# Kernel optimization log

Measured on AMD Instinct MI355X. Metric: run time of the kernel, lower is better.

Reference implementation:

```python
import jax, jax.numpy as jnp
import numpy as np

B, C, D, H = 2, 1024, 1024, 16
DH = D // H
EPS = 1e-8


def setup_inputs() -> dict:
    key = jax.random.key(0)
    ks = jax.random.split(key, 12)
    s = 0.02
    return {
        "x": jax.random.normal(ks[0], (B, C, D), dtype=jnp.float32),
        "rms_w": jnp.ones((C, D), dtype=jnp.float32),
        "rms_b": jnp.zeros((C, D), dtype=jnp.float32),
        "Wqkv": jax.random.normal(ks[1], (3 * D, D), dtype=jnp.float32) * s,
        "Wout": jax.random.normal(ks[2], (D, D), dtype=jnp.float32) * s,
        "bout": jnp.zeros((D,), dtype=jnp.float32),
        "Wf": jax.random.normal(ks[3], (D, D), dtype=jnp.float32) * s,
        "bf": jnp.zeros((D,), dtype=jnp.float32),
        "Ww": jax.random.normal(ks[4], (D, D), dtype=jnp.float32) * s,
        "bw": jnp.zeros((D,), dtype=jnp.float32),
        "Wv": jax.random.normal(ks[5], (D, D), dtype=jnp.float32) * s,
        "bv": jnp.zeros((D,), dtype=jnp.float32),
        "beta": jnp.ones((1,), dtype=jnp.float32),
    }


def _rope_cos_sin(C, dh):
    # faithful to source: theta = 10000 ** (-2*(i-1)/dh), i in [0, dh//2)
    i = jnp.arange(dh // 2, dtype=jnp.float32)
    theta = 10000.0 ** (-2.0 * (i - 1.0) / dh)            # [dh//2]
    ang = jnp.arange(C, dtype=jnp.float32)[:, None] * theta  # [C, dh//2]
    return jnp.cos(ang), jnp.sin(ang)


def _rotate(t, cos, sin):
    # equivalent to einsum('bhci,cij->bhcj', t, R) with the source R
    ev, od = t[..., 0::2], t[..., 1::2]          # [B,H,C,dh//2]
    out_ev = ev * cos + od * sin
    out_od = -ev * sin + od * cos
    return jnp.stack([out_ev, out_od], axis=-1).reshape(t.shape)


def _rmsnorm(x, w, b):
    rms = jnp.sqrt(jnp.mean(x * x, axis=-1, keepdims=True) + EPS)
    return w * (x / rms) + b


def _attention(x, Wqkv, Wout, bout):
    qkv = x @ Wqkv.T                               # [B,C,3D]
    q, k, v = jnp.split(qkv, 3, axis=-1)
    def heads(t):
        return t.reshape(B, C, H, DH).transpose(0, 2, 1, 3)  # [B,H,C,dh]
    q, k, v = heads(q), heads(k), heads(v)
    cos, sin = _rope_cos_sin(C, DH)
    qr = _rotate(q, cos, sin)
    kr = _rotate(k, cos, sin)
    scale = 1.0 / jnp.sqrt(jnp.float32(DH))
    num = jnp.exp(jnp.einsum('bhid,bhjd->bhij', qr, kr) * scale)
    den = jnp.sum(jnp.exp(jnp.einsum('bhid,bhjd->bhij', q, k) * scale),
                  axis=-1, keepdims=True)
    attn = num / den
    mask = jnp.tril(jnp.ones((C, C), dtype=bool))
    attn = jnp.where(mask[None, None], attn, 0.0)
    y = attn @ v                                   # [B,H,C,dh]
    y = y.transpose(0, 2, 1, 3).reshape(B, C, D)
    return y @ Wout.T + bout


def _ffn(x, Wf, bf, Ww, bw, Wv, bv, beta):
    h = x @ Wf.T + bf
    wx = h @ Ww.T + bw
    swish = wx * jax.nn.sigmoid(beta * wx)
    return swish * (h @ Wv.T + bv)


def reference(x, rms_w, rms_b, Wqkv, Wout, bout, Wf, bf, Ww, bw, Wv, bv, beta):
    # dropout p is identity in eval mode
    x = _rmsnorm(x, rms_w, rms_b)
    x = x + _attention(x, Wqkv, Wout, bout)
    x = _rmsnorm(x, rms_w, rms_b)   # same shared RMSNorm module applied twice
    x = x + _ffn(x, Wf, bf, Ww, bw, Wv, bv, beta)
    return x
```

## Files before the change

### kernel.cpp

```cpp
#include <hip/hip_runtime.h>
#include <math.h>

#define B_ 2
#define C_ 1024
#define D_ 1024
#define H_ 16
#define DH_ 64
#define EPSF 1e-8f
#define BK 32

typedef __bf16 bf16;
typedef __attribute__((ext_vector_type(4))) __bf16 bf16x4;
typedef __attribute__((ext_vector_type(8))) __bf16 bf16x8;
typedef __attribute__((ext_vector_type(4))) float f32x4;

__device__ inline f32x4 mfma16(bf16x8 a, bf16x8 b, f32x4 c) {
  return __builtin_amdgcn_mfma_f32_16x16x32_bf16(a, b, c, 0, 0, 0);
}

__device__ inline void async16(const bf16* g, bf16* l) {
  __builtin_amdgcn_global_load_lds((const __attribute__((address_space(1))) void*)g,
                                   (__attribute__((address_space(3))) void*)l, 16, 0, 0);
}

__global__ __launch_bounds__(256) void cvt_all_kernel(const float* __restrict__ wqkv,
                                                      const float* __restrict__ wout,
                                                      const float* __restrict__ wf,
                                                      const float* __restrict__ www,
                                                      const float* __restrict__ wv,
                                                      bf16* __restrict__ dst) {
  int seg = blockIdx.x >> 10;
  int local = (blockIdx.x & 1023) * 1024 + threadIdx.x * 4;
  const float* src = seg < 3 ? wqkv + (size_t)seg * (D_ * D_)
                   : seg == 3 ? wout : seg == 4 ? wf : seg == 5 ? www : wv;
  float4 v = *(const float4*)(src + local);
  bf16x4 o;
  o[0] = (bf16)v.x; o[1] = (bf16)v.y; o[2] = (bf16)v.z; o[3] = (bf16)v.w;
  *(bf16x4*)(dst + (size_t)seg * (D_ * D_) + local) = o;
}

__global__ __launch_bounds__(256) void rmsnorm_f32_kernel(const float* __restrict__ x,
                                                          const float* __restrict__ w,
                                                          const float* __restrict__ b,
                                                          bf16* __restrict__ out) {
  int row = blockIdx.x;
  int c = row & (C_ - 1);
  int t = threadIdx.x;
  float4 xv = *(const float4*)(x + (size_t)row * D_ + t * 4);
  float ss = xv.x * xv.x + xv.y * xv.y + xv.z * xv.z + xv.w * xv.w;
#pragma unroll
  for (int m = 1; m < 64; m <<= 1) ss += __shfl_xor(ss, m, 64);
  __shared__ float red[4];
  if ((t & 63) == 0) red[t >> 6] = ss;
  __syncthreads();
  float tot = red[0] + red[1] + red[2] + red[3];
  float inv = rsqrtf(tot * (1.0f / D_) + EPSF);
  float4 wv = *(const float4*)(w + (size_t)c * D_ + t * 4);
  float4 bv = *(const float4*)(b + (size_t)c * D_ + t * 4);
  bf16x4 ov;
  ov[0] = (bf16)(wv.x * (xv.x * inv) + bv.x);
  ov[1] = (bf16)(wv.y * (xv.y * inv) + bv.y);
  ov[2] = (bf16)(wv.z * (xv.z * inv) + bv.z);
  ov[3] = (bf16)(wv.w * (xv.w * inv) + bv.w);
  *(bf16x4*)(out + (size_t)row * D_ + t * 4) = ov;
}

__global__ __launch_bounds__(256) void rmsnorm_bf16_kernel(const bf16* __restrict__ x,
                                                           const float* __restrict__ w,
                                                           const float* __restrict__ b,
                                                           bf16* __restrict__ out) {
  int row = blockIdx.x;
  int c = row & (C_ - 1);
  int t = threadIdx.x;
  bf16x4 xv = *(const bf16x4*)(x + (size_t)row * D_ + t * 4);
  float f0 = (float)xv[0], f1 = (float)xv[1], f2 = (float)xv[2], f3 = (float)xv[3];
  float ss = f0 * f0 + f1 * f1 + f2 * f2 + f3 * f3;
#pragma unroll
  for (int m = 1; m < 64; m <<= 1) ss += __shfl_xor(ss, m, 64);
  __shared__ float red[4];
  if ((t & 63) == 0) red[t >> 6] = ss;
  __syncthreads();
  float tot = red[0] + red[1] + red[2] + red[3];
  float inv = rsqrtf(tot * (1.0f / D_) + EPSF);
  float4 wv = *(const float4*)(w + (size_t)c * D_ + t * 4);
  float4 bv = *(const float4*)(b + (size_t)c * D_ + t * 4);
  bf16x4 ov;
  ov[0] = (bf16)(wv.x * (f0 * inv) + bv.x);
  ov[1] = (bf16)(wv.y * (f1 * inv) + bv.y);
  ov[2] = (bf16)(wv.z * (f2 * inv) + bv.z);
  ov[3] = (bf16)(wv.w * (f3 * inv) + bv.w);
  *(bf16x4*)(out + (size_t)row * D_ + t * 4) = ov;
}

template <int BMt, int BNt>
__global__ __launch_bounds__(256) void gemm_lds(const bf16* __restrict__ A,
                                                const bf16* __restrict__ W,
                                                const float* __restrict__ bias,
                                                const bf16* __restrict__ R,
                                                bf16* __restrict__ Cout,
                                                int M, int N, int K) {
  constexpr int MT = BMt / 32;
  constexpr int NT = BNt / 32;
  __shared__ bf16 sa[BMt * BK];
  __shared__ bf16 sb[BNt * BK];
  int t = threadIdx.x, l = t & 63, w = t >> 6;
  int m0 = blockIdx.y * BMt;
  int n0 = blockIdx.x * BNt;
  int wm = (w >> 1) * (BMt / 2), wn = (w & 1) * (BNt / 2);
  int lm = l & 15, lq = l >> 4;
  f32x4 acc[MT][NT] = {};

  for (int k0 = 0; k0 < K; k0 += BK) {
    __syncthreads();
#pragma unroll
    for (int p = 0; p < BMt / 64; ++p) {
      int lin = p * 256 + t;
      async16(A + (size_t)(m0 + (lin >> 2)) * K + k0 + (lin & 3) * 8, sa + lin * 8);
    }
#pragma unroll
    for (int p = 0; p < BNt / 64; ++p) {
      int lin = p * 256 + t;
      async16(W + (size_t)(n0 + (lin >> 2)) * K + k0 + (lin & 3) * 8, sb + lin * 8);
    }
    __syncthreads();
    bf16x8 af[MT], bfr[NT];
#pragma unroll
    for (int mt = 0; mt < MT; ++mt)
      af[mt] = *(const bf16x8*)(sa + (wm + mt * 16 + lm) * BK + lq * 8);
#pragma unroll
    for (int nt = 0; nt < NT; ++nt)
      bfr[nt] = *(const bf16x8*)(sb + (wn + nt * 16 + lm) * BK + lq * 8);
#pragma unroll
    for (int mt = 0; mt < MT; ++mt)
#pragma unroll
      for (int nt = 0; nt < NT; ++nt)
        acc[mt][nt] = mfma16(af[mt], bfr[nt], acc[mt][nt]);
  }
#pragma unroll
  for (int mt = 0; mt < MT; ++mt)
#pragma unroll
    for (int nt = 0; nt < NT; ++nt) {
      int col = n0 + wn + nt * 16 + lm;
      float bb = bias ? bias[col] : 0.0f;
#pragma unroll
      for (int r = 0; r < 4; ++r) {
        int row = m0 + wm + mt * 16 + lq * 4 + r;
        float v = acc[mt][nt][r] + bb;
        if (R) v += (float)R[(size_t)row * N + col];
        Cout[(size_t)row * N + col] = (bf16)v;
      }
    }
}

__global__ __launch_bounds__(256) void gemm_ffn_kernel(const bf16* __restrict__ A,
                                                       const bf16* __restrict__ Ww,
                                                       const bf16* __restrict__ Wv,
                                                       const float* __restrict__ bw,
                                                       const float* __restrict__ bv,
                                                       const bf16* __restrict__ x3,
                                                       const float* __restrict__ beta_p,
                                                       float* __restrict__ out) {
  __shared__ bf16 sa[64 * BK];
  __shared__ bf16 sb1[64 * BK];
  __shared__ bf16 sb2[64 * BK];
  int t = threadIdx.x, l = t & 63, w = t >> 6;
  int m0 = blockIdx.y * 64, n0 = blockIdx.x * 64;
  int wm = (w >> 1) * 32, wn = (w & 1) * 32;
  int lm = l & 15, lq = l >> 4;
  float beta = beta_p[0];
  f32x4 acc1[2][2] = {}, acc2[2][2] = {};

  for (int k0 = 0; k0 < D_; k0 += BK) {
    __syncthreads();
    async16(A + (size_t)(m0 + (t >> 2)) * D_ + k0 + (t & 3) * 8, sa + t * 8);
    async16(Ww + (size_t)(n0 + (t >> 2)) * D_ + k0 + (t & 3) * 8, sb1 + t * 8);
    async16(Wv + (size_t)(n0 + (t >> 2)) * D_ + k0 + (t & 3) * 8, sb2 + t * 8);
    __syncthreads();
    bf16x8 af[2], b1f[2], b2f[2];
#pragma unroll
    for (int mt = 0; mt < 2; ++mt)
      af[mt] = *(const bf16x8*)(sa + (wm + mt * 16 + lm) * BK + lq * 8);
#pragma unroll
    for (int nt = 0; nt < 2; ++nt) {
      b1f[nt] = *(const bf16x8*)(sb1 + (wn + nt * 16 + lm) * BK + lq * 8);
      b2f[nt] = *(const bf16x8*)(sb2 + (wn + nt * 16 + lm) * BK + lq * 8);
    }
#pragma unroll
    for (int mt = 0; mt < 2; ++mt)
#pragma unroll
      for (int nt = 0; nt < 2; ++nt) {
        acc1[mt][nt] = mfma16(af[mt], b1f[nt], acc1[mt][nt]);
        acc2[mt][nt] = mfma16(af[mt], b2f[nt], acc2[mt][nt]);
      }
  }
#pragma unroll
  for (int mt = 0; mt < 2; ++mt)
#pragma unroll
    for (int nt = 0; nt < 2; ++nt) {
      int col = n0 + wn + nt * 16 + lm;
      float bbw = bw[col], bbv = bv[col];
#pragma unroll
      for (int r = 0; r < 4; ++r) {
        int row = m0 + wm + mt * 16 + lq * 4 + r;
        float z = acc1[mt][nt][r] + bbw;
        float g = acc2[mt][nt][r] + bbv;
        float sw = z / (1.0f + __expf(-beta * z));
        out[(size_t)row * D_ + col] = (float)x3[(size_t)row * D_ + col] + sw * g;
      }
    }
}

__global__ __launch_bounds__(256) void prep_kernel(const bf16* __restrict__ qkv,
                                                   bf16* __restrict__ qr,
                                                   bf16* __restrict__ kr,
                                                   bf16* __restrict__ vt) {
  __shared__ bf16 tile[64][65];
  int t = threadIdx.x;
  int blk = blockIdx.x;
  int ct = blk & 15;
  int h = (blk >> 4) & 15;
  int b = blk >> 8;
  int c0 = ct * 64;
  size_t hb = (size_t)((b * H_ + h) * C_);

#pragma unroll
  for (int p = 0; p < 2; ++p) {
    int row = p * 32 + (t >> 3);
    int col = (t & 7) * 8;
    int c = c0 + row;
    size_t gq = (size_t)(b * C_ + c) * (3 * D_) + h * DH_ + col;
    bf16x8 qv = *(const bf16x8*)(qkv + gq);
    bf16x8 kv = *(const bf16x8*)(qkv + gq + D_);
    bf16x8 qo, ko;
#pragma unroll
    for (int j = 0; j < 4; ++j) {
      int i = (col >> 1) + j;
      float theta = exp2f(-13.287712379549449f * (2.0f * ((float)i - 1.0f) / 64.0f));
      float ang = (float)c * theta;
      float sv = __sinf(ang), cv = __cosf(ang);
      float qe = (float)qv[2 * j], qo_ = (float)qv[2 * j + 1];
      float ke = (float)kv[2 * j], ko_ = (float)kv[2 * j + 1];
      qo[2 * j] = (bf16)(qe * cv + qo_ * sv);
      qo[2 * j + 1] = (bf16)(qo_ * cv - qe * sv);
      ko[2 * j] = (bf16)(ke * cv + ko_ * sv);
      ko[2 * j + 1] = (bf16)(ko_ * cv - ke * sv);
    }
    *(bf16x8*)(qr + (hb + c) * DH_ + col) = qo;
    *(bf16x8*)(kr + (hb + c) * DH_ + col) = ko;
  }

#pragma unroll
  for (int p = 0; p < 16; ++p) {
    int lin = p * 256 + t;
    int cl = lin >> 6, dh = lin & 63;
    tile[dh][cl] = qkv[(size_t)(b * C_ + c0 + cl) * (3 * D_) + 2 * D_ + h * DH_ + dh];
  }
  __syncthreads();
  size_t vbase = (size_t)((b * H_ + h) * DH_) * C_;
#pragma unroll
  for (int p = 0; p < 16; ++p) {
    int lin = p * 256 + t;
    int dh = lin >> 6, cl = lin & 63;
    vt[vbase + (size_t)dh * C_ + c0 + cl] = tile[dh][cl];
  }
}

__global__ __launch_bounds__(256) void attn_kernel(const bf16* __restrict__ qkv,
                                                   const bf16* __restrict__ qr,
                                                   const bf16* __restrict__ kr,
                                                   const bf16* __restrict__ vt,
                                                   float* __restrict__ yp,
                                                   float* __restrict__ dp) {
  __shared__ bf16 sk[64 * 72];
  __shared__ bf16 skr[64 * 72];
  __shared__ bf16 sv[64 * 72];
  __shared__ bf16 pl[4][16 * 72];
  int t = threadIdx.x, l = t & 63, w = t >> 6;
  int blk = blockIdx.x;
  int half = blk & 1;
  int it = (blk >> 1) & 15;
  int h = (blk >> 5) & 15;
  int b = blk >> 9;
  int i_base = it * 64 + w * 16;
  int lm = l & 15, lq = l >> 4;
  const float scale = 0.125f;
  int jf = half << 9;

  size_t hq = (size_t)h * DH_;
  size_t qrow = (size_t)(b * C_ + i_base + lm) * (3 * D_) + hq;
  size_t hb = (size_t)((b * H_ + h) * C_);
  bf16x8 qp[2], qrf[2];
#pragma unroll
  for (int kk = 0; kk < 2; ++kk) {
    qp[kk] = *(const bf16x8*)(qkv + qrow + kk * 32 + lq * 8);
    qrf[kk] = *(const bf16x8*)(qr + (hb + i_base + lm) * DH_ + kk * 32 + lq * 8);
  }

  float den[4] = {0.f, 0.f, 0.f, 0.f};
  f32x4 yacc[4] = {};
  int i_max = i_base + 15;
  size_t kbase = (size_t)(b * C_) * (3 * D_) + D_ + hq;
  size_t krbase = hb * DH_;
  size_t vtbase = (size_t)((b * H_ + h) * DH_) * C_;
  int sr = t >> 3;
  int sc = (t & 7) * 8;

  int4 pk0, pk1, pkr0, pkr1, pv0, pv1;
#define FETCH_TILE(J0)                                                               \
  pk0 = *(const int4*)(qkv + kbase + (size_t)((J0) + sr) * (3 * D_) + sc);           \
  pk1 = *(const int4*)(qkv + kbase + (size_t)((J0) + 32 + sr) * (3 * D_) + sc);      \
  pkr0 = *(const int4*)(kr + krbase + (size_t)((J0) + sr) * DH_ + sc);               \
  pkr1 = *(const int4*)(kr + krbase + (size_t)((J0) + 32 + sr) * DH_ + sc);          \
  pv0 = *(const int4*)(vt + vtbase + (size_t)sr * C_ + (J0) + sc);                   \
  pv1 = *(const int4*)(vt + vtbase + (size_t)(32 + sr) * C_ + (J0) + sc);

  FETCH_TILE(jf)

  for (int j0 = jf; j0 < jf + 512; j0 += 64) {
    __syncthreads();
    *(int4*)(sk + sr * 72 + sc) = pk0;
    *(int4*)(sk + (32 + sr) * 72 + sc) = pk1;
    *(int4*)(skr + sr * 72 + sc) = pkr0;
    *(int4*)(skr + (32 + sr) * 72 + sc) = pkr1;
    *(int4*)(sv + sr * 72 + sc) = pv0;
    *(int4*)(sv + (32 + sr) * 72 + sc) = pv1;
    __syncthreads();
    if (j0 + 64 < jf + 512) {
      FETCH_TILE(j0 + 64)
    }
#pragma unroll
    for (int js = 0; js < 64; js += 16) {
      bf16x8 kf0 = *(const bf16x8*)(sk + (js + lm) * 72 + lq * 8);
      bf16x8 kf1 = *(const bf16x8*)(sk + (js + lm) * 72 + 32 + lq * 8);
      f32x4 s = {0.f, 0.f, 0.f, 0.f};
      s = mfma16(qp[0], kf0, s);
      s = mfma16(qp[1], kf1, s);
#pragma unroll
      for (int r = 0; r < 4; ++r) den[r] += __expf(s[r] * scale);
    }
    if (j0 <= i_max) {
#pragma unroll
      for (int js = 0; js < 64; js += 16) {
        bf16x8 kf0 = *(const bf16x8*)(skr + (js + lm) * 72 + lq * 8);
        bf16x8 kf1 = *(const bf16x8*)(skr + (js + lm) * 72 + 32 + lq * 8);
        f32x4 s = {0.f, 0.f, 0.f, 0.f};
        s = mfma16(qrf[0], kf0, s);
        s = mfma16(qrf[1], kf1, s);
#pragma unroll
        for (int r = 0; r < 4; ++r) {
          int jg = j0 + js + lm;
          int ig = i_base + lq * 4 + r;
          float p = (jg <= ig) ? __expf(s[r] * scale) : 0.0f;
          pl[w][(lq * 4 + r) * 72 + js + lm] = (bf16)p;
        }
      }
      __builtin_amdgcn_wave_barrier();
      bf16x8 pf0 = *(const bf16x8*)(pl[w] + lm * 72 + lq * 8);
      bf16x8 pf1 = *(const bf16x8*)(pl[w] + lm * 72 + 32 + lq * 8);
#pragma unroll
      for (int tt = 0; tt < 4; ++tt) {
        bf16x8 vf0 = *(const bf16x8*)(sv + (tt * 16 + lm) * 72 + lq * 8);
        bf16x8 vf1 = *(const bf16x8*)(sv + (tt * 16 + lm) * 72 + 32 + lq * 8);
        yacc[tt] = mfma16(pf0, vf0, mfma16(pf1, vf1, yacc[tt]));
      }
      __builtin_amdgcn_wave_barrier();
    }
  }
#undef FETCH_TILE
#pragma unroll
  for (int r = 0; r < 4; ++r) {
    float d = den[r];
    d += __shfl_xor(d, 1, 64);
    d += __shfl_xor(d, 2, 64);
    d += __shfl_xor(d, 4, 64);
    d += __shfl_xor(d, 8, 64);
    if (lm == 0) dp[(size_t)blk * 64 + w * 16 + lq * 4 + r] = d;
  }
  size_t yb = (size_t)blk * 4096;
#pragma unroll
  for (int tt = 0; tt < 4; ++tt)
#pragma unroll
    for (int r = 0; r < 4; ++r)
      yp[yb + (size_t)(w * 16 + lq * 4 + r) * 64 + tt * 16 + lm] = yacc[tt][r];
}

__global__ __launch_bounds__(256) void combine_kernel(const float* __restrict__ yp,
                                                      const float* __restrict__ dp,
                                                      bf16* __restrict__ y) {
  int cb = blockIdx.x;
  int it = cb & 15;
  int h = (cb >> 4) & 15;
  int b = cb >> 8;
  int t = threadIdx.x;
  int row = t >> 2;
  int cg = (t & 3) * 16;
  size_t p0 = (size_t)(cb * 2) * 4096 + (size_t)row * 64 + cg;
  size_t p1 = p0 + 4096;
  float inv = 1.0f / (dp[(size_t)(cb * 2) * 64 + row] + dp[(size_t)(cb * 2 + 1) * 64 + row]);
  bf16x8 o0, o1;
#pragma unroll
  for (int c = 0; c < 8; ++c) o0[c] = (bf16)((yp[p0 + c] + yp[p1 + c]) * inv);
#pragma unroll
  for (int c = 0; c < 8; ++c) o1[c] = (bf16)((yp[p0 + 8 + c] + yp[p1 + 8 + c]) * inv);
  size_t ob = (size_t)(b * C_ + it * 64 + row) * D_ + h * DH_ + cg;
  *(bf16x8*)(y + ob) = o0;
  *(bf16x8*)(y + ob + 8) = o1;
}

extern "C" void kernel_launch(void* const* d_in, const int* in_sizes, int n_in,
                              void* d_out, int out_size, void* d_ws, size_t ws_size,
                              hipStream_t stream) {
  const float* x = (const float*)d_in[0];
  const float* rms_w = (const float*)d_in[1];
  const float* rms_b = (const float*)d_in[2];
  const float* Wqkv = (const float*)d_in[3];
  const float* Wout = (const float*)d_in[4];
  const float* bout = (const float*)d_in[5];
  const float* Wf = (const float*)d_in[6];
  const float* bfp = (const float*)d_in[7];
  const float* Ww = (const float*)d_in[8];
  const float* bw = (const float*)d_in[9];
  const float* Wv = (const float*)d_in[10];
  const float* bv = (const float*)d_in[11];
  const float* beta = (const float*)d_in[12];
  float* out = (float*)d_out;

  bf16* ws = (bf16*)d_ws;
  const size_t DD = (size_t)D_ * D_;
  const size_t MC = (size_t)B_ * C_;
  bf16* wb = ws;
  bf16* x1 = ws + 7 * DD;
  bf16* qkv = ws + 9 * DD;
  bf16* qr = ws + 15 * DD;
  bf16* kr = ws + 17 * DD;
  bf16* vt = ws + 19 * DD;
  bf16* x2 = ws + 21 * DD;
  bf16* x3 = ws + 23 * DD;
  bf16* hbuf = ws + 25 * DD;
  float* yp = (float*)(ws + 28 * DD);
  float* dp = yp + (size_t)1024 * 4096;
  bf16* y = (bf16*)d_out;

  cvt_all_kernel<<<7 * 1024, 256, 0, stream>>>(Wqkv, Wout, Wf, Ww, Wv, wb);
  rmsnorm_f32_kernel<<<MC, 256, 0, stream>>>(x, rms_w, rms_b, x1);
  gemm_lds<128, 64><<<dim3(3 * D_ / 64, MC / 128), 256, 0, stream>>>(
      x1, wb, nullptr, nullptr, qkv, MC, 3 * D_, D_);
  prep_kernel<<<B_ * H_ * (C_ / 64), 256, 0, stream>>>(qkv, qr, kr, vt);
  attn_kernel<<<B_ * H_ * 16 * 2, 256, 0, stream>>>(qkv, qr, kr, vt, yp, dp);
  combine_kernel<<<B_ * H_ * 16, 256, 0, stream>>>(yp, dp, y);
  gemm_lds<64, 64><<<dim3(D_ / 64, MC / 64), 256, 0, stream>>>(
      y, wb + 3 * DD, bout, x1, x2, MC, D_, D_);
  rmsnorm_bf16_kernel<<<MC, 256, 0, stream>>>(x2, rms_w, rms_b, x3);
  gemm_lds<64, 64><<<dim3(D_ / 64, MC / 64), 256, 0, stream>>>(
      x3, wb + 4 * DD, bfp, nullptr, hbuf, MC, D_, D_);
  gemm_ffn_kernel<<<dim3(D_ / 64, MC / 64), 256, 0, stream>>>(
      hbuf, wb + 5 * DD, wb + 6 * DD, bw, bv, x3, beta, out);
}
```

Before: 233.8 us.

## Fuse RoPE and V transpose into attention; merge weight cast with RMSNorm

Removes the separate prep kernel. The attention kernel now computes rotated Q in registers, rotates each K tile while staging it into LDS, and writes V transposed into LDS straight from the qkv buffer, so the qr/kr/vt intermediates are no longer written and read back from global memory. The weight-cast kernel and the first RMSNorm are merged into one launch to save a launch boundary. In exchange, sincos work is repeated for every tile, so each K row is rotated once per query block that uses it. The scalar transposed LDS writes for V may cause bank conflicts.

```diff
diff --git a/kernel.cpp b/kernel.cpp
--- a/kernel.cpp
+++ b/kernel.cpp
@@ -23,46 +23,51 @@
                                    (__attribute__((address_space(3))) void*)l, 16, 0, 0);
 }
 
-__global__ __launch_bounds__(256) void cvt_all_kernel(const float* __restrict__ wqkv,
+__device__ inline float rope_theta(float i) {
+  return exp2f(-13.287712379549449f * (2.0f * (i - 1.0f) * (1.0f / 64.0f)));
+}
+
+__global__ __launch_bounds__(256) void cvt_rms_kernel(const float* __restrict__ wqkv,
                                                       const float* __restrict__ wout,
                                                       const float* __restrict__ wf,
                                                       const float* __restrict__ www,
                                                       const float* __restrict__ wv,
-                                                      bf16* __restrict__ dst) {
-  int seg = blockIdx.x >> 10;
-  int local = (blockIdx.x & 1023) * 1024 + threadIdx.x * 4;
-  const float* src = seg < 3 ? wqkv + (size_t)seg * (D_ * D_)
-                   : seg == 3 ? wout : seg == 4 ? wf : seg == 5 ? www : wv;
-  float4 v = *(const float4*)(src + local);
-  bf16x4 o;
-  o[0] = (bf16)v.x; o[1] = (bf16)v.y; o[2] = (bf16)v.z; o[3] = (bf16)v.w;
-  *(bf16x4*)(dst + (size_t)seg * (D_ * D_) + local) = o;
-}
-
-__global__ __launch_bounds__(256) void rmsnorm_f32_kernel(const float* __restrict__ x,
-                                                          const float* __restrict__ w,
-                                                          const float* __restrict__ b,
-                                                          bf16* __restrict__ out) {
-  int row = blockIdx.x;
+                                                      bf16* __restrict__ wdst,
+                                                      const float* __restrict__ x,
+                                                      const float* __restrict__ rw,
+                                                      const float* __restrict__ rb,
+                                                      bf16* __restrict__ xout) {
+  __shared__ float red[4];
+  int t = threadIdx.x;
+  if (blockIdx.x < 7 * 1024) {
+    int seg = blockIdx.x >> 10;
+    int local = (blockIdx.x & 1023) * 1024 + t * 4;
+    const float* src = seg < 3 ? wqkv + (size_t)seg * (D_ * D_)
+                     : seg == 3 ? wout : seg == 4 ? wf : seg == 5 ? www : wv;
+    float4 v = *(const float4*)(src + local);
+    bf16x4 o;
+    o[0] = (bf16)v.x; o[1] = (bf16)v.y; o[2] = (bf16)v.z; o[3] = (bf16)v.w;
+    *(bf16x4*)(wdst + (size_t)seg * (D_ * D_) + local) = o;
+    return;
+  }
+  int row = blockIdx.x - 7 * 1024;
   int c = row & (C_ - 1);
-  int t = threadIdx.x;
   float4 xv = *(const float4*)(x + (size_t)row * D_ + t * 4);
   float ss = xv.x * xv.x + xv.y * xv.y + xv.z * xv.z + xv.w * xv.w;
 #pragma unroll
   for (int m = 1; m < 64; m <<= 1) ss += __shfl_xor(ss, m, 64);
-  __shared__ float red[4];
   if ((t & 63) == 0) red[t >> 6] = ss;
   __syncthreads();
   float tot = red[0] + red[1] + red[2] + red[3];
   float inv = rsqrtf(tot * (1.0f / D_) + EPSF);
-  float4 wv = *(const float4*)(w + (size_t)c * D_ + t * 4);
-  float4 bv = *(const float4*)(b + (size_t)c * D_ + t * 4);
+  float4 wv4 = *(const float4*)(rw + (size_t)c * D_ + t * 4);
+  float4 bv4 = *(const float4*)(rb + (size_t)c * D_ + t * 4);
   bf16x4 ov;
-  ov[0] = (bf16)(wv.x * (xv.x * inv) + bv.x);
-  ov[1] = (bf16)(wv.y * (xv.y * inv) + bv.y);
-  ov[2] = (bf16)(wv.z * (xv.z * inv) + bv.z);
-  ov[3] = (bf16)(wv.w * (xv.w * inv) + bv.w);
-  *(bf16x4*)(out + (size_t)row * D_ + t * 4) = ov;
+  ov[0] = (bf16)(wv4.x * (xv.x * inv) + bv4.x);
+  ov[1] = (bf16)(wv4.y * (xv.y * inv) + bv4.y);
+  ov[2] = (bf16)(wv4.z * (xv.z * inv) + bv4.z);
+  ov[3] = (bf16)(wv4.w * (xv.w * inv) + bv4.w);
+  *(bf16x4*)(xout + (size_t)row * D_ + t * 4) = ov;
 }
 
 __global__ __launch_bounds__(256) void rmsnorm_bf16_kernel(const bf16* __restrict__ x,
@@ -210,65 +215,7 @@
     }
 }
 
-__global__ __launch_bounds__(256) void prep_kernel(const bf16* __restrict__ qkv,
-                                                   bf16* __restrict__ qr,
-                                                   bf16* __restrict__ kr,
-                                                   bf16* __restrict__ vt) {
-  __shared__ bf16 tile[64][65];
-  int t = threadIdx.x;
-  int blk = blockIdx.x;
-  int ct = blk & 15;
-  int h = (blk >> 4) & 15;
-  int b = blk >> 8;
-  int c0 = ct * 64;
-  size_t hb = (size_t)((b * H_ + h) * C_);
-
-#pragma unroll
-  for (int p = 0; p < 2; ++p) {
-    int row = p * 32 + (t >> 3);
-    int col = (t & 7) * 8;
-    int c = c0 + row;
-    size_t gq = (size_t)(b * C_ + c) * (3 * D_) + h * DH_ + col;
-    bf16x8 qv = *(const bf16x8*)(qkv + gq);
-    bf16x8 kv = *(const bf16x8*)(qkv + gq + D_);
-    bf16x8 qo, ko;
-#pragma unroll
-    for (int j = 0; j < 4; ++j) {
-      int i = (col >> 1) + j;
-      float theta = exp2f(-13.287712379549449f * (2.0f * ((float)i - 1.0f) / 64.0f));
-      float ang = (float)c * theta;
-      float sv = __sinf(ang), cv = __cosf(ang);
-      float qe = (float)qv[2 * j], qo_ = (float)qv[2 * j + 1];
-      float ke = (float)kv[2 * j], ko_ = (float)kv[2 * j + 1];
-      qo[2 * j] = (bf16)(qe * cv + qo_ * sv);
-      qo[2 * j + 1] = (bf16)(qo_ * cv - qe * sv);
-      ko[2 * j] = (bf16)(ke * cv + ko_ * sv);
-      ko[2 * j + 1] = (bf16)(ko_ * cv - ke * sv);
-    }
-    *(bf16x8*)(qr + (hb + c) * DH_ + col) = qo;
-    *(bf16x8*)(kr + (hb + c) * DH_ + col) = ko;
-  }
-
-#pragma unroll
-  for (int p = 0; p < 16; ++p) {
-    int lin = p * 256 + t;
-    int cl = lin >> 6, dh = lin & 63;
-    tile[dh][cl] = qkv[(size_t)(b * C_ + c0 + cl) * (3 * D_) + 2 * D_ + h * DH_ + dh];
-  }
-  __syncthreads();
-  size_t vbase = (size_t)((b * H_ + h) * DH_) * C_;
-#pragma unroll
-  for (int p = 0; p < 16; ++p) {
-    int lin = p * 256 + t;
-    int dh = lin >> 6, cl = lin & 63;
-    vt[vbase + (size_t)dh * C_ + c0 + cl] = tile[dh][cl];
-  }
-}
-
 __global__ __launch_bounds__(256) void attn_kernel(const bf16* __restrict__ qkv,
-                                                   const bf16* __restrict__ qr,
-                                                   const bf16* __restrict__ kr,
-                                                   const bf16* __restrict__ vt,
                                                    float* __restrict__ yp,
                                                    float* __restrict__ dp) {
   __shared__ bf16 sk[64 * 72];
@@ -288,31 +235,41 @@
 
   size_t hq = (size_t)h * DH_;
   size_t qrow = (size_t)(b * C_ + i_base + lm) * (3 * D_) + hq;
-  size_t hb = (size_t)((b * H_ + h) * C_);
   bf16x8 qp[2], qrf[2];
+  float cq = (float)(i_base + lm);
 #pragma unroll
   for (int kk = 0; kk < 2; ++kk) {
     qp[kk] = *(const bf16x8*)(qkv + qrow + kk * 32 + lq * 8);
-    qrf[kk] = *(const bf16x8*)(qr + (hb + i_base + lm) * DH_ + kk * 32 + lq * 8);
+#pragma unroll
+    for (int j = 0; j < 4; ++j) {
+      float ip = (float)(kk * 16 + lq * 4 + j);
+      float ang = cq * rope_theta(ip);
+      float sv_, cv_;
+      __sincosf(ang, &sv_, &cv_);
+      float qe = (float)qp[kk][2 * j], qo = (float)qp[kk][2 * j + 1];
+      qrf[kk][2 * j] = (bf16)(qe * cv_ + qo * sv_);
+      qrf[kk][2 * j + 1] = (bf16)(qo * cv_ - qe * sv_);
+    }
   }
 
   float den[4] = {0.f, 0.f, 0.f, 0.f};
   f32x4 yacc[4] = {};
   int i_max = i_base + 15;
   size_t kbase = (size_t)(b * C_) * (3 * D_) + D_ + hq;
-  size_t krbase = hb * DH_;
-  size_t vtbase = (size_t)((b * H_ + h) * DH_) * C_;
+  size_t vbase = (size_t)(b * C_) * (3 * D_) + 2 * D_ + hq;
   int sr = t >> 3;
   int sc = (t & 7) * 8;
-
-  int4 pk0, pk1, pkr0, pkr1, pv0, pv1;
-#define FETCH_TILE(J0)                                                               \
-  pk0 = *(const int4*)(qkv + kbase + (size_t)((J0) + sr) * (3 * D_) + sc);           \
-  pk1 = *(const int4*)(qkv + kbase + (size_t)((J0) + 32 + sr) * (3 * D_) + sc);      \
-  pkr0 = *(const int4*)(kr + krbase + (size_t)((J0) + sr) * DH_ + sc);               \
-  pkr1 = *(const int4*)(kr + krbase + (size_t)((J0) + 32 + sr) * DH_ + sc);          \
-  pv0 = *(const int4*)(vt + vtbase + (size_t)sr * C_ + (J0) + sc);                   \
-  pv1 = *(const int4*)(vt + vtbase + (size_t)(32 + sr) * C_ + (J0) + sc);
+  float th0 = rope_theta((float)((sc >> 1) + 0));
+  float th1 = rope_theta((float)((sc >> 1) + 1));
+  float th2 = rope_theta((float)((sc >> 1) + 2));
+  float th3 = rope_theta((float)((sc >> 1) + 3));
+
+  int4 pk0, pk1, pv0, pv1;
+#define FETCH_TILE(J0)                                                          \
+  pk0 = *(const int4*)(qkv + kbase + (size_t)((J0) + sr) * (3 * D_) + sc);      \
+  pk1 = *(const int4*)(qkv + kbase + (size_t)((J0) + 32 + sr) * (3 * D_) + sc); \
+  pv0 = *(const int4*)(qkv + vbase + (size_t)((J0) + sr) * (3 * D_) + sc);      \
+  pv1 = *(const int4*)(qkv + vbase + (size_t)((J0) + 32 + sr) * (3 * D_) + sc);
 
   FETCH_TILE(jf)
 
@@ -320,10 +277,35 @@
     __syncthreads();
     *(int4*)(sk + sr * 72 + sc) = pk0;
     *(int4*)(sk + (32 + sr) * 72 + sc) = pk1;
-    *(int4*)(skr + sr * 72 + sc) = pkr0;
-    *(int4*)(skr + (32 + sr) * 72 + sc) = pkr1;
-    *(int4*)(sv + sr * 72 + sc) = pv0;
-    *(int4*)(sv + (32 + sr) * 72 + sc) = pv1;
+    {
+      bf16x8 k0 = *(bf16x8*)&pk0, k1 = *(bf16x8*)&pk1;
+      bf16x8 r0, r1;
+      float a, s_, c_;
+      float jg0 = (float)(j0 + sr), jg1 = (float)(j0 + 32 + sr);
+#define ROT(KV, RV, JG, TH, J)                                       \
+  a = (JG)*TH;                                                       \
+  __sincosf(a, &s_, &c_);                                            \
+  {                                                                  \
+    float e = (float)KV[2 * J], o = (float)KV[2 * J + 1];            \
+    RV[2 * J] = (bf16)(e * c_ + o * s_);                             \
+    RV[2 * J + 1] = (bf16)(o * c_ - e * s_);                         \
+  }
+      ROT(k0, r0, jg0, th0, 0) ROT(k0, r0, jg0, th1, 1)
+      ROT(k0, r0, jg0, th2, 2) ROT(k0, r0, jg0, th3, 3)
+      ROT(k1, r1, jg1, th0, 0) ROT(k1, r1, jg1, th1, 1)
+      ROT(k1, r1, jg1, th2, 2) ROT(k1, r1, jg1, th3, 3)
+#undef ROT
+      *(int4*)(skr + sr * 72 + sc) = *(int4*)&r0;
+      *(int4*)(skr + (32 + sr) * 72 + sc) = *(int4*)&r1;
+    }
+    {
+      bf16x8 v0 = *(bf16x8*)&pv0, v1 = *(bf16x8*)&pv1;
+#pragma unroll
+      for (int e = 0; e < 8; ++e) {
+        sv[(sc + e) * 72 + sr] = v0[e];
+        sv[(sc + e) * 72 + 32 + sr] = v1[e];
+      }
+    }
     __syncthreads();
     if (j0 + 64 < jf + 512) {
       FETCH_TILE(j0 + 64)
@@ -431,22 +413,18 @@
   bf16* wb = ws;
   bf16* x1 = ws + 7 * DD;
   bf16* qkv = ws + 9 * DD;
-  bf16* qr = ws + 15 * DD;
-  bf16* kr = ws + 17 * DD;
-  bf16* vt = ws + 19 * DD;
-  bf16* x2 = ws + 21 * DD;
-  bf16* x3 = ws + 23 * DD;
-  bf16* hbuf = ws + 25 * DD;
-  float* yp = (float*)(ws + 28 * DD);
+  bf16* x2 = ws + 15 * DD;
+  bf16* x3 = ws + 17 * DD;
+  bf16* hbuf = ws + 19 * DD;
+  float* yp = (float*)(ws + 22 * DD);
   float* dp = yp + (size_t)1024 * 4096;
   bf16* y = (bf16*)d_out;
 
-  cvt_all_kernel<<<7 * 1024, 256, 0, stream>>>(Wqkv, Wout, Wf, Ww, Wv, wb);
-  rmsnorm_f32_kernel<<<MC, 256, 0, stream>>>(x, rms_w, rms_b, x1);
+  cvt_rms_kernel<<<7 * 1024 + MC, 256, 0, stream>>>(Wqkv, Wout, Wf, Ww, Wv, wb, x, rms_w,
+                                                    rms_b, x1);
   gemm_lds<128, 64><<<dim3(3 * D_ / 64, MC / 128), 256, 0, stream>>>(
       x1, wb, nullptr, nullptr, qkv, MC, 3 * D_, D_);
-  prep_kernel<<<B_ * H_ * (C_ / 64), 256, 0, stream>>>(qkv, qr, kr, vt);
-  attn_kernel<<<B_ * H_ * 16 * 2, 256, 0, stream>>>(qkv, qr, kr, vt, yp, dp);
+  attn_kernel<<<B_ * H_ * 16 * 2, 256, 0, stream>>>(qkv, yp, dp);
   combine_kernel<<<B_ * H_ * 16, 256, 0, stream>>>(yp, dp, y);
   gemm_lds<64, 64><<<dim3(D_ / 64, MC / 64), 256, 0, stream>>>(
       y, wb + 3 * DD, bout, x1, x2, MC, D_, D_);
```

Result: slower. 238.7 us (+2.1%).
